# Performance work log

Hardware: AMD Instinct MI355X
Metric: run time of the kernel (lower is better)

The kernel has to match this reference:

```python
import jax, jax.numpy as jnp
import numpy as np


def _quantize(x, weight):
    # x: (B, D, H, W); weight: (D, K)
    B, D, H, W = x.shape
    K = weight.shape[1]
    xf = x.reshape(B, D, H * W)  # (B, D, N)
    x2 = jnp.sum(xf * xf, axis=1)                      # (B, N)
    cross = jnp.einsum('bdn,dk->bnk', xf, weight)       # (B, N, K)
    e2 = jnp.sum(weight * weight, axis=0)               # (K,)
    d2 = x2[..., None] - 2.0 * cross + e2               # (B, N, K)
    argmin = jnp.argmin(d2, axis=-1)                    # (B, N)
    # gather codes: (B, N, D) -> (B, D, N) -> (B, D, H, W)
    quant = weight.T[argmin]                            # (B, N, D)
    result = jnp.transpose(quant, (0, 2, 1)).reshape(B, D, H, W)
    return result, argmin.reshape(B, H, W)


def setup_inputs() -> dict:
    key = jax.random.key(0)
    k1, k2 = jax.random.split(key)
    x = jax.random.normal(k1, (32, 256, 32, 32), dtype=jnp.float32)
    weight = jax.random.uniform(k2, (256, 512), dtype=jnp.float32)  # torch.rand init
    return {"x": x, "weight": weight}


def reference(x, weight):
    result, argmin = _quantize(x, weight)
    return result, argmin
```

## Files before the change

### kernel.cpp

```cpp
#include <hip/hip_runtime.h>

typedef __attribute__((ext_vector_type(8))) short bf16x8;
typedef __attribute__((ext_vector_type(16))) float f32x16;

__device__ __forceinline__ bool lex_lt(float av, int ai, float bv, int bi) {
  return av < bv || (av == bv && ai < bi);
}

__device__ __forceinline__ unsigned bf16_rne(float v) {
  unsigned u = __float_as_uint(v);
  return (u + 0x7fffu + ((u >> 16) & 1u)) >> 16;
}

__device__ __forceinline__ unsigned pk_bf16(float a, float b) {
  return bf16_rne(a) | (bf16_rne(b) << 16);
}

__global__ __launch_bounds__(256) void vq_pre(
    const float* __restrict__ w, float* __restrict__ e2,
    short* __restrict__ wtil, float* __restrict__ wT) {
  int blk = blockIdx.x;
  if (blk < 64) {
    int gid = blk * 256 + threadIdx.x;
    int n  = gid & 511;
    int kg = gid >> 9;
    bf16x8 hv, lv;
    float vv[8];
#pragma unroll
    for (int j = 0; j < 8; ++j) {
      float v = w[(kg * 8 + j) * 512 + n];
      vv[j] = v;
      unsigned h = bf16_rne(v);
      float hf = __uint_as_float(h << 16);
      unsigned l = bf16_rne(v - hf);
      hv[j] = (short)h;
      lv[j] = (short)l;
    }
    short* dst = wtil + (size_t)gid * 8;
    *(bf16x8*)dst = hv;
    *(bf16x8*)(dst + 131072) = lv;
    if (wT) {
      float* p = wT + (size_t)n * 256 + kg * 8;
      *(float4*)p       = make_float4(vv[0], vv[1], vv[2], vv[3]);
      *(float4*)(p + 4) = make_float4(vv[4], vv[5], vv[6], vv[7]);
    }
  } else {
    int t = (blk - 64) * 256 + threadIdx.x;
    int k = t >> 2;
    int part = t & 3;
    double s = 0.0;
#pragma unroll 8
    for (int d = part * 64; d < part * 64 + 64; ++d) {
      double v = (double)w[d * 512 + k];
      s = fma(v, v, s);
    }
    s += __shfl_xor(s, 1);
    s += __shfl_xor(s, 2);
    if (part == 0) e2[k] = (float)s;
  }
}

__global__ __launch_bounds__(512, 2) void vq_main(
    const float* __restrict__ x, const float* __restrict__ w,
    const float* __restrict__ e2g, const short* __restrict__ wtil,
    const float* __restrict__ wT,
    float* __restrict__ out, float* __restrict__ arg_out) {
  __shared__ __align__(16) char arena[151552];
  short* xh   = (short*)arena;
  short* xl   = (short*)(arena + 65536);
  float* e2s  = (float*)(arena + 131072);
  float* tv1  = (float*)(arena + 133120);
  float* tv2  = (float*)(arena + 137216);
  int*   ti1  = (int*)(arena + 141312);
  int*   ti2  = (int*)(arena + 145408);
  int*   p1S  = (int*)(arena + 149504);
  int*   p2S  = (int*)(arena + 150016);
  int*   needS= (int*)(arena + 150528);
  int*   rpickS=(int*)(arena + 151040);
  float* gbuf = (float*)arena;

  const int tid = threadIdx.x;
  const int b  = blockIdx.x >> 3;
  const int n0 = (blockIdx.x & 7) << 7;
  const float* xbase = x + (size_t)b * 262144 + n0;

  const int n4  = tid & 31;
  const int kgp = tid >> 5;

  auto load8 = [&](int kg, float4* v) {
#pragma unroll
    for (int j = 0; j < 8; ++j)
      v[j] = *(const float4*)(xbase + (size_t)(kg * 8 + j) * 1024 + (n4 << 2));
  };
  auto convert_write = [&](int kg, const float4* v) {
#pragma unroll
    for (int i = 0; i < 4; ++i) {
      int m = (n4 << 2) + i;
      union { int w4[4]; bf16x8 v8; } H, L;
#pragma unroll
      for (int jj = 0; jj < 4; ++jj) {
        float a = (i == 0) ? v[2*jj].x : (i == 1) ? v[2*jj].y : (i == 2) ? v[2*jj].z : v[2*jj].w;
        float c = (i == 0) ? v[2*jj+1].x : (i == 1) ? v[2*jj+1].y : (i == 2) ? v[2*jj+1].z : v[2*jj+1].w;
        unsigned hu = pk_bf16(a, c);
        float haf = __uint_as_float(hu << 16);
        float hcf = __uint_as_float(hu & 0xffff0000u);
        unsigned lu = pk_bf16(a - haf, c - hcf);
        H.w4[jj] = (int)hu;
        L.w4[jj] = (int)lu;
      }
      int off = (m << 8) + ((kg ^ (m & 7)) << 3);
      *(bf16x8*)&xh[off] = H.v8;
      *(bf16x8*)&xl[off] = L.v8;
    }
  };

  {
    float4 v0[8];
    load8(kgp, v0);
    convert_write(kgp, v0);
    e2s[tid] = e2g[tid];
  }
  __syncthreads();

  const int lane = tid & 63;
  const int wv   = tid >> 6;
  const int ln   = lane & 31;
  const int half = lane >> 5;
  const int wb   = wv << 6;

  f32x16 acc[2][4];
#pragma unroll
  for (int ct = 0; ct < 2; ++ct)
#pragma unroll
    for (int pt = 0; pt < 4; ++pt)
#pragma unroll
      for (int r = 0; r < 16; ++r) acc[ct][pt][r] = 0.f;

  const int asw = ln & 7;
  const int abase = ln << 8;

  int bofs[2];
#pragma unroll
  for (int ct = 0; ct < 2; ++ct) bofs[ct] = (wb + (ct << 5) + ln) << 3;

  bf16x8 pch[2], pcl[2];
#pragma unroll
  for (int ct = 0; ct < 2; ++ct) {
    const short* p = wtil + (half << 12) + bofs[ct];
    pch[ct] = *(const bf16x8*)p;
    pcl[ct] = *(const bf16x8*)(p + 131072);
  }

  auto kstep = [&](int ch) {
    const int kg = (ch << 1) + half;
    const int ao = abase + ((kg ^ asw) << 3);
    bf16x8 xf[4], xg[4];
#pragma unroll
    for (int pt = 0; pt < 4; ++pt) {
      xf[pt] = *(const bf16x8*)&xh[ao + (pt << 13)];
      xg[pt] = *(const bf16x8*)&xl[ao + (pt << 13)];
    }
    bf16x8 cfh[2], cfl[2];
#pragma unroll
    for (int ct = 0; ct < 2; ++ct) { cfh[ct] = pch[ct]; cfl[ct] = pcl[ct]; }
    if (ch < 15) {
      const int kgn = ((ch + 1) << 1) + half;
#pragma unroll
      for (int ct = 0; ct < 2; ++ct) {
        const short* p = wtil + (kgn << 12) + bofs[ct];
        pch[ct] = *(const bf16x8*)p;
        pcl[ct] = *(const bf16x8*)(p + 131072);
      }
    }
#pragma unroll
    for (int ct = 0; ct < 2; ++ct)
#pragma unroll
      for (int pt = 0; pt < 4; ++pt) {
        acc[ct][pt] = __builtin_amdgcn_mfma_f32_32x32x16_bf16(cfh[ct], xf[pt], acc[ct][pt], 0, 0, 0);
        acc[ct][pt] = __builtin_amdgcn_mfma_f32_32x32x16_bf16(cfh[ct], xg[pt], acc[ct][pt], 0, 0, 0);
        acc[ct][pt] = __builtin_amdgcn_mfma_f32_32x32x16_bf16(cfl[ct], xf[pt], acc[ct][pt], 0, 0, 0);
      }
  };

  float4 vx[8];
  load8(kgp + 16, vx);
  kstep(0); kstep(1); kstep(2); kstep(3);
  convert_write(kgp + 16, vx);
  kstep(4); kstep(5); kstep(6); kstep(7);
  __syncthreads();
  kstep(8); kstep(9); kstep(10); kstep(11);
  kstep(12); kstep(13); kstep(14); kstep(15);

  float e2r[2][16];
#pragma unroll
  for (int ct = 0; ct < 2; ++ct)
#pragma unroll
    for (int r = 0; r < 16; ++r)
      e2r[ct][r] = e2s[wb + (ct << 5) + (r & 3) + ((r >> 2) << 3) + (half << 2)];

#pragma unroll
  for (int pt = 0; pt < 4; ++pt) {
    float v1 = 3.4e38f, v2 = 3.4e38f;
    int i1 = 0x7fffffff, i2 = 0x7fffffff;
#pragma unroll
    for (int ct = 0; ct < 2; ++ct) {
#pragma unroll
      for (int r = 0; r < 16; ++r) {
        int k = wb + (ct << 5) + (r & 3) + ((r >> 2) << 3) + (half << 2);
        float s = fmaf(-2.f, acc[ct][pt][r], e2r[ct][r]);
        if (lex_lt(s, k, v1, i1)) { v2 = v1; i2 = i1; v1 = s; i1 = k; }
        else if (lex_lt(s, k, v2, i2)) { v2 = s; i2 = k; }
      }
    }
    {
      float ov1 = __shfl_xor(v1, 32);
      int   oi1 = __shfl_xor(i1, 32);
      float ov2 = __shfl_xor(v2, 32);
      int   oi2 = __shfl_xor(i2, 32);
      bool aFirst = lex_lt(v1, i1, ov1, oi1);
      float nv1 = aFirst ? v1 : ov1;  int ni1 = aFirst ? i1 : oi1;
      float cv  = aFirst ? ov1 : v1;  int ci  = aFirst ? oi1 : i1;
      float sv  = aFirst ? v2 : ov2;  int si  = aFirst ? i2 : oi2;
      bool cFirst = lex_lt(cv, ci, sv, si);
      v1 = nv1; i1 = ni1;
      v2 = cFirst ? cv : sv; i2 = cFirst ? ci : si;
    }
    if (half == 0) {
      int s = (wv << 7) + (pt << 5) + ln;
      tv1[s] = v1; ti1[s] = i1; tv2[s] = v2; ti2[s] = i2;
    }
  }
  __syncthreads();

  if (tid < 128) {
    int row = tid;
    float v1 = 3.4e38f, v2 = 3.4e38f;
    int i1 = 0x7fffffff, i2 = 0x7fffffff;
#pragma unroll
    for (int wvv = 0; wvv < 8; ++wvv) {
      int s = (wvv << 7) + row;
      float a1 = tv1[s]; int ai = ti1[s];
      float a2 = tv2[s]; int bi = ti2[s];
      if (lex_lt(a1, ai, v1, i1)) { v2 = v1; i2 = i1; v1 = a1; i1 = ai; }
      else if (lex_lt(a1, ai, v2, i2)) { v2 = a1; i2 = ai; }
      if (lex_lt(a2, bi, v1, i1)) { v2 = v1; i2 = i1; v1 = a2; i1 = bi; }
      else if (lex_lt(a2, bi, v2, i2)) { v2 = a2; i2 = bi; }
    }
    p1S[row] = i1; p2S[row] = i2;
    needS[row] = (v2 - v1 < 0.01f) ? 1 : 0;
    rpickS[row] = i1;
  }
  __syncthreads();

  for (int t = 0; t < 16; ++t) {
    int row = (t << 3) + wv;
    if (needS[row]) {
      int i1 = p1S[row], i2 = p2S[row];
      const float* xp = x + (size_t)b * 262144 + n0 + row;
      double s1 = 0.0, s2 = 0.0;
      int k0 = lane << 2;
#pragma unroll
      for (int i = 0; i < 4; ++i) {
        int k = k0 + i;
        double xv = (double)xp[(size_t)k * 1024];
        double w1 = (double)w[k * 512 + i1];
        double w2 = (double)w[k * 512 + i2];
        double t1 = xv - w1, t2 = xv - w2;
        s1 = fma(t1, t1, s1);
        s2 = fma(t2, t2, s2);
      }
#pragma unroll
      for (int off = 32; off >= 1; off >>= 1) {
        s1 += __shfl_xor(s1, off);
        s2 += __shfl_xor(s2, off);
      }
      if (lane == 0 && (s2 < s1 || (s2 == s1 && i2 < i1))) rpickS[row] = i2;
    }
  }
  __syncthreads();

  if (tid < 128) arg_out[b * 1024 + n0 + tid] = (float)rpickS[tid];

  if (wT) {
    {
      const int pos  = tid >> 2;
      const int dseg = tid & 3;
      const float* wrow = wT + (size_t)rpickS[pos] * 256;
#pragma unroll
      for (int j = 0; j < 16; ++j) {
        int d0 = (j << 4) + (dseg << 2);
        float4 v = *(const float4*)(wrow + d0);
        gbuf[(d0 + 0) * 132 + pos] = v.x;
        gbuf[(d0 + 1) * 132 + pos] = v.y;
        gbuf[(d0 + 2) * 132 + pos] = v.z;
        gbuf[(d0 + 3) * 132 + pos] = v.w;
      }
    }
    __syncthreads();
    {
      const int nn0 = (tid & 31) << 2;
      const int d0g = tid >> 5;
      float* obase = out + (size_t)b * 262144 + n0 + nn0;
#pragma unroll
      for (int dg = 0; dg < 16; ++dg) {
        int d = d0g + (dg << 4);
        float4 o = *(const float4*)&gbuf[d * 132 + nn0];
        *(float4*)(obase + (size_t)d * 1024) = o;
      }
    }
  } else {
    const int nn0 = (tid & 31) << 2;
    const int d0g = tid >> 5;
    int pk0 = rpickS[nn0], pk1 = rpickS[nn0 + 1], pk2 = rpickS[nn0 + 2], pk3 = rpickS[nn0 + 3];
    float* obase = out + (size_t)b * 262144 + n0 + nn0;
#pragma unroll
    for (int dg = 0; dg < 16; ++dg) {
      int d = d0g + (dg << 4);
      const float* wr = w + d * 512;
      float4 o = make_float4(wr[pk0], wr[pk1], wr[pk2], wr[pk3]);
      *(float4*)(obase + (size_t)d * 1024) = o;
    }
  }
}

extern "C" void kernel_launch(void* const* d_in, const int* in_sizes, int n_in,
                              void* d_out, int out_size, void* d_ws, size_t ws_size,
                              hipStream_t stream) {
  const float* x = (const float*)d_in[0];
  const float* w = (const float*)d_in[1];
  float* out  = (float*)d_out;
  float* argf = out + 8388608;
  float* e2   = (float*)d_ws;
  short* wtil = (short*)((char*)d_ws + 2048);
  size_t need = 2048 + 524288 + 524288;
  float* wT   = (ws_size >= need) ? (float*)((char*)d_ws + 2048 + 524288) : nullptr;

  vq_pre<<<72, 256, 0, stream>>>(w, e2, wtil, wT);
  vq_main<<<256, 512, 0, stream>>>(x, w, e2, wtil, wT, out, argf);
}
```

Before: 121.2 us.

## Double block to 1024 threads with one codebook tile per wave

The main kernel now launches 1024 threads per block, so each of 16 waves handles 32 codes instead of 64. This halves the accumulator registers per wave and adds waves for latency hiding. The x tile is loaded in one pass, which removes the overlapped second half-load, and a second XOR term is added to the LDS swizzle to cut bank conflicts. The reduction scratch now aliases the x staging area to shrink shared memory, and the epilogue loops are re-split for the larger block. In exchange, each wave re-reads the x fragments from LDS for half as many codes, which doubles LDS read traffic, and the reduction across waves gets deeper.

```diff
diff --git a/kernel.cpp b/kernel.cpp
--- a/kernel.cpp
+++ b/kernel.cpp
@@ -60,23 +60,23 @@
   }
 }
 
-__global__ __launch_bounds__(512, 2) void vq_main(
+__global__ __launch_bounds__(1024, 4) void vq_main(
     const float* __restrict__ x, const float* __restrict__ w,
     const float* __restrict__ e2g, const short* __restrict__ wtil,
     const float* __restrict__ wT,
     float* __restrict__ out, float* __restrict__ arg_out) {
-  __shared__ __align__(16) char arena[151552];
+  __shared__ __align__(16) char arena[137216];
   short* xh   = (short*)arena;
   short* xl   = (short*)(arena + 65536);
   float* e2s  = (float*)(arena + 131072);
-  float* tv1  = (float*)(arena + 133120);
-  float* tv2  = (float*)(arena + 137216);
-  int*   ti1  = (int*)(arena + 141312);
-  int*   ti2  = (int*)(arena + 145408);
-  int*   p1S  = (int*)(arena + 149504);
-  int*   p2S  = (int*)(arena + 150016);
-  int*   needS= (int*)(arena + 150528);
-  int*   rpickS=(int*)(arena + 151040);
+  float* tv1  = (float*)arena;
+  float* tv2  = (float*)(arena + 8192);
+  int*   ti1  = (int*)(arena + 16384);
+  int*   ti2  = (int*)(arena + 24576);
+  int*   p1S  = (int*)(arena + 135168);
+  int*   p2S  = (int*)(arena + 135680);
+  int*   needS= (int*)(arena + 136192);
+  int*   rpickS=(int*)(arena + 136704);
   float* gbuf = (float*)arena;
 
   const int tid = threadIdx.x;
@@ -84,15 +84,14 @@
   const int n0 = (blockIdx.x & 7) << 7;
   const float* xbase = x + (size_t)b * 262144 + n0;
 
-  const int n4  = tid & 31;
-  const int kgp = tid >> 5;
-
-  auto load8 = [&](int kg, float4* v) {
+  {
+    if (tid < 512) e2s[tid] = e2g[tid];
+    const int n4  = tid & 31;
+    const int kgp = tid >> 5;
+    float4 v[8];
 #pragma unroll
     for (int j = 0; j < 8; ++j)
-      v[j] = *(const float4*)(xbase + (size_t)(kg * 8 + j) * 1024 + (n4 << 2));
-  };
-  auto convert_write = [&](int kg, const float4* v) {
+      v[j] = *(const float4*)(xbase + (size_t)(kgp * 8 + j) * 1024 + (n4 << 2));
 #pragma unroll
     for (int i = 0; i < 4; ++i) {
       int m = (n4 << 2) + i;
@@ -108,17 +107,11 @@
         H.w4[jj] = (int)hu;
         L.w4[jj] = (int)lu;
       }
-      int off = (m << 8) + ((kg ^ (m & 7)) << 3);
+      int slot = kgp ^ (m & 7) ^ ((m >> 3) & 7);
+      int off = (m << 8) + (slot << 3);
       *(bf16x8*)&xh[off] = H.v8;
       *(bf16x8*)&xl[off] = L.v8;
     }
-  };
-
-  {
-    float4 v0[8];
-    load8(kgp, v0);
-    convert_write(kgp, v0);
-    e2s[tid] = e2g[tid];
   }
   __syncthreads();
 
@@ -126,91 +119,62 @@
   const int wv   = tid >> 6;
   const int ln   = lane & 31;
   const int half = lane >> 5;
-  const int wb   = wv << 6;
-
-  f32x16 acc[2][4];
-#pragma unroll
-  for (int ct = 0; ct < 2; ++ct)
-#pragma unroll
-    for (int pt = 0; pt < 4; ++pt)
-#pragma unroll
-      for (int r = 0; r < 16; ++r) acc[ct][pt][r] = 0.f;
-
-  const int asw = ln & 7;
+  const int wb   = wv << 5;
+
+  f32x16 acc[4];
+#pragma unroll
+  for (int pt = 0; pt < 4; ++pt)
+#pragma unroll
+    for (int r = 0; r < 16; ++r) acc[pt][r] = 0.f;
+
+  const int sw0   = ((ln & 7) ^ (ln >> 3)) << 3;
   const int abase = ln << 8;
-
-  int bofs[2];
-#pragma unroll
-  for (int ct = 0; ct < 2; ++ct) bofs[ct] = (wb + (ct << 5) + ln) << 3;
-
-  bf16x8 pch[2], pcl[2];
-#pragma unroll
-  for (int ct = 0; ct < 2; ++ct) {
-    const short* p = wtil + (half << 12) + bofs[ct];
-    pch[ct] = *(const bf16x8*)p;
-    pcl[ct] = *(const bf16x8*)(p + 131072);
+  const int bofs  = (wb + ln) << 3;
+
+  bf16x8 pch, pcl;
+  {
+    const short* p = wtil + (half << 12) + bofs;
+    pch = *(const bf16x8*)p;
+    pcl = *(const bf16x8*)(p + 131072);
   }
 
   auto kstep = [&](int ch) {
     const int kg = (ch << 1) + half;
-    const int ao = abase + ((kg ^ asw) << 3);
-    bf16x8 xf[4], xg[4];
+    bf16x8 cfh = pch, cfl = pcl;
+    if (ch < 15) {
+      const short* p = wtil + ((((ch + 1) << 1) + half) << 12) + bofs;
+      pch = *(const bf16x8*)p;
+      pcl = *(const bf16x8*)(p + 131072);
+    }
+    const int kbase = (kg << 3) ^ sw0;
 #pragma unroll
     for (int pt = 0; pt < 4; ++pt) {
-      xf[pt] = *(const bf16x8*)&xh[ao + (pt << 13)];
-      xg[pt] = *(const bf16x8*)&xl[ao + (pt << 13)];
-    }
-    bf16x8 cfh[2], cfl[2];
-#pragma unroll
-    for (int ct = 0; ct < 2; ++ct) { cfh[ct] = pch[ct]; cfl[ct] = pcl[ct]; }
-    if (ch < 15) {
-      const int kgn = ((ch + 1) << 1) + half;
-#pragma unroll
-      for (int ct = 0; ct < 2; ++ct) {
-        const short* p = wtil + (kgn << 12) + bofs[ct];
-        pch[ct] = *(const bf16x8*)p;
-        pcl[ct] = *(const bf16x8*)(p + 131072);
-      }
-    }
-#pragma unroll
-    for (int ct = 0; ct < 2; ++ct)
-#pragma unroll
-      for (int pt = 0; pt < 4; ++pt) {
-        acc[ct][pt] = __builtin_amdgcn_mfma_f32_32x32x16_bf16(cfh[ct], xf[pt], acc[ct][pt], 0, 0, 0);
-        acc[ct][pt] = __builtin_amdgcn_mfma_f32_32x32x16_bf16(cfh[ct], xg[pt], acc[ct][pt], 0, 0, 0);
-        acc[ct][pt] = __builtin_amdgcn_mfma_f32_32x32x16_bf16(cfl[ct], xf[pt], acc[ct][pt], 0, 0, 0);
-      }
+      const int ao = abase + (pt << 13) + (kbase ^ ((pt & 1) << 5));
+      bf16x8 xf = *(const bf16x8*)&xh[ao];
+      bf16x8 xg = *(const bf16x8*)&xl[ao];
+      acc[pt] = __builtin_amdgcn_mfma_f32_32x32x16_bf16(cfh, xf, acc[pt], 0, 0, 0);
+      acc[pt] = __builtin_amdgcn_mfma_f32_32x32x16_bf16(cfh, xg, acc[pt], 0, 0, 0);
+      acc[pt] = __builtin_amdgcn_mfma_f32_32x32x16_bf16(cfl, xf, acc[pt], 0, 0, 0);
+    }
   };
 
-  float4 vx[8];
-  load8(kgp + 16, vx);
-  kstep(0); kstep(1); kstep(2); kstep(3);
-  convert_write(kgp + 16, vx);
-  kstep(4); kstep(5); kstep(6); kstep(7);
-  __syncthreads();
-  kstep(8); kstep(9); kstep(10); kstep(11);
+  kstep(0);  kstep(1);  kstep(2);  kstep(3);
+  kstep(4);  kstep(5);  kstep(6);  kstep(7);
+  kstep(8);  kstep(9);  kstep(10); kstep(11);
   kstep(12); kstep(13); kstep(14); kstep(15);
 
-  float e2r[2][16];
-#pragma unroll
-  for (int ct = 0; ct < 2; ++ct)
-#pragma unroll
-    for (int r = 0; r < 16; ++r)
-      e2r[ct][r] = e2s[wb + (ct << 5) + (r & 3) + ((r >> 2) << 3) + (half << 2)];
+  __syncthreads();
 
 #pragma unroll
   for (int pt = 0; pt < 4; ++pt) {
     float v1 = 3.4e38f, v2 = 3.4e38f;
     int i1 = 0x7fffffff, i2 = 0x7fffffff;
 #pragma unroll
-    for (int ct = 0; ct < 2; ++ct) {
-#pragma unroll
-      for (int r = 0; r < 16; ++r) {
-        int k = wb + (ct << 5) + (r & 3) + ((r >> 2) << 3) + (half << 2);
-        float s = fmaf(-2.f, acc[ct][pt][r], e2r[ct][r]);
-        if (lex_lt(s, k, v1, i1)) { v2 = v1; i2 = i1; v1 = s; i1 = k; }
-        else if (lex_lt(s, k, v2, i2)) { v2 = s; i2 = k; }
-      }
+    for (int r = 0; r < 16; ++r) {
+      int k = wb + (r & 3) + ((r >> 2) << 3) + (half << 2);
+      float s = fmaf(-2.f, acc[pt][r], e2s[k]);
+      if (lex_lt(s, k, v1, i1)) { v2 = v1; i2 = i1; v1 = s; i1 = k; }
+      else if (lex_lt(s, k, v2, i2)) { v2 = s; i2 = k; }
     }
     {
       float ov1 = __shfl_xor(v1, 32);
@@ -237,7 +201,7 @@
     float v1 = 3.4e38f, v2 = 3.4e38f;
     int i1 = 0x7fffffff, i2 = 0x7fffffff;
 #pragma unroll
-    for (int wvv = 0; wvv < 8; ++wvv) {
+    for (int wvv = 0; wvv < 16; ++wvv) {
       int s = (wvv << 7) + row;
       float a1 = tv1[s]; int ai = ti1[s];
       float a2 = tv2[s]; int bi = ti2[s];
@@ -252,8 +216,8 @@
   }
   __syncthreads();
 
-  for (int t = 0; t < 16; ++t) {
-    int row = (t << 3) + wv;
+  for (int t = 0; t < 8; ++t) {
+    int row = (t << 4) + wv;
     if (needS[row]) {
       int i1 = p1S[row], i2 = p2S[row];
       const float* xp = x + (size_t)b * 262144 + n0 + row;
@@ -283,12 +247,12 @@
 
   if (wT) {
     {
-      const int pos  = tid >> 2;
-      const int dseg = tid & 3;
+      const int pos  = tid >> 3;
+      const int dseg = tid & 7;
       const float* wrow = wT + (size_t)rpickS[pos] * 256;
 #pragma unroll
-      for (int j = 0; j < 16; ++j) {
-        int d0 = (j << 4) + (dseg << 2);
+      for (int j = 0; j < 8; ++j) {
+        int d0 = (j << 5) + (dseg << 2);
         float4 v = *(const float4*)(wrow + d0);
         gbuf[(d0 + 0) * 132 + pos] = v.x;
         gbuf[(d0 + 1) * 132 + pos] = v.y;
@@ -302,8 +266,8 @@
       const int d0g = tid >> 5;
       float* obase = out + (size_t)b * 262144 + n0 + nn0;
 #pragma unroll
-      for (int dg = 0; dg < 16; ++dg) {
-        int d = d0g + (dg << 4);
+      for (int dg = 0; dg < 8; ++dg) {
+        int d = d0g + (dg << 5);
         float4 o = *(const float4*)&gbuf[d * 132 + nn0];
         *(float4*)(obase + (size_t)d * 1024) = o;
       }
@@ -314,8 +278,8 @@
     int pk0 = rpickS[nn0], pk1 = rpickS[nn0 + 1], pk2 = rpickS[nn0 + 2], pk3 = rpickS[nn0 + 3];
     float* obase = out + (size_t)b * 262144 + n0 + nn0;
 #pragma unroll
-    for (int dg = 0; dg < 16; ++dg) {
-      int d = d0g + (dg << 4);
+    for (int dg = 0; dg < 8; ++dg) {
+      int d = d0g + (dg << 5);
       const float* wr = w + d * 512;
       float4 o = make_float4(wr[pk0], wr[pk1], wr[pk2], wr[pk3]);
       *(float4*)(obase + (size_t)d * 1024) = o;
@@ -336,5 +300,5 @@
   float* wT   = (ws_size >= need) ? (float*)((char*)d_ws + 2048 + 524288) : nullptr;
 
   vq_pre<<<72, 256, 0, stream>>>(w, e2, wtil, wT);
-  vq_main<<<256, 512, 0, stream>>>(x, w, e2, wtil, wT, out, argf);
-}
+  vq_main<<<256, 1024, 0, stream>>>(x, w, e2, wtil, wT, out, argf);
+}
```

Measured after the change: 119.9 us. Within noise of the previous version (-1.0%).
